# Kernel tuning notes

Measured on AMD Instinct MI355X. Metric: run time of the kernel, lower is better.

Reference implementation:

```python
import jax, jax.numpy as jnp
import numpy as np

FSIZE = 5
PAD = FSIZE // 2


def _conv(mosaick, filts):
    # mosaick [B,1,H,W], filts [f,f,K] -> responses [B,K,H,W].
    # Cross-correlation with edge-clamped boundary (Halide clamp semantics).
    x = jnp.pad(mosaick, ((0, 0), (0, 0), (PAD, PAD), (PAD, PAD)), mode='edge')
    k = jnp.transpose(filts, (2, 0, 1))[:, None, :, :]  # [K,1,f,f] OIHW
    return jax.lax.conv_general_dilated(
        x, k, window_strides=(1, 1), padding='VALID',
        dimension_numbers=('NCHW', 'OIHW', 'NCHW'))


def setup_inputs() -> dict:
    key = jax.random.key(0)
    k1, k2, k3 = jax.random.split(key, 3)
    B, H, W, K, f = 16, 512, 512, 8, FSIZE
    std = 1.0 / (f * f)  # matches normal_(0, 1/(fsize*fsize))
    return {
        'mosaick': jax.random.normal(k1, (B, 1, H, W), dtype=jnp.float32),
        'sel_filts': jax.random.normal(k2, (f, f, K), dtype=jnp.float32) * std,
        'green_filts': jax.random.normal(k3, (f, f, K), dtype=jnp.float32) * std,
    }


def reference(mosaick, sel_filts, green_filts):
    # Per-pixel soft filter selection over K candidate green-interpolation filters.
    sel = _conv(mosaick, sel_filts)      # [B,K,H,W] selection scores
    grn = _conv(mosaick, green_filts)    # [B,K,H,W] candidate green estimates
    w = jax.nn.softmax(sel, axis=1)      # softmax over filter bank
    interp = jnp.sum(w * grn, axis=1, keepdims=True)  # [B,1,H,W]
    # GRBG Bayer: green where row parity == col parity; copy known greens.
    H, W = mosaick.shape[-2], mosaick.shape[-1]
    yy = jnp.arange(H)[:, None]
    xx = jnp.arange(W)[None, :]
    is_green = (yy % 2) == (xx % 2)      # [H,W] bool
    # Output green channel only (module returns output[:, 1:2, ...]).
    return jnp.where(is_green, mosaick, interp)
```

## Files before the change

kernel.cpp:

```cpp
#include <hip/hip_runtime.h>


typedef float f32x4 __attribute__((ext_vector_type(4)));
typedef short s16x8 __attribute__((ext_vector_type(8)));

#define HH 512
#define WW 512
#define TW 64
#define TH 16
#define RS 80
#define NROW 20
#define NEL 72

__device__ __forceinline__ unsigned short bf16rne(float x) {
    unsigned u = __float_as_uint(x);
    u += 0x7fffu + ((u >> 16) & 1u);
    return (unsigned short)(u >> 16);
}
__device__ __forceinline__ int pk2(float hi, float lo) {
    return (int)((((unsigned)bf16rne(hi)) << 16) | (unsigned)bf16rne(lo));
}
__device__ __forceinline__ float hi16(int v) { return __uint_as_float(((unsigned)v) & 0xffff0000u); }
__device__ __forceinline__ float lo16(int v) { return __uint_as_float(((unsigned)v) << 16); }

__global__ __launch_bounds__(256) void demosaick_kernel(
    const float* __restrict__ mos,
    const float* __restrict__ sf,
    const float* __restrict__ gf,
    float* __restrict__ out)
{
    __shared__ alignas(16) unsigned short tileS[NROW * RS];

    const int tid   = threadIdx.x;
    const int bx    = blockIdx.x;
    const int by    = blockIdx.y;
    const int bimg  = blockIdx.z;
    const int tileX = bx * TW;
    const int tileY = by * TH;
    const float* img = mos + (size_t)bimg * HH * WW;

    const bool interior = (bx >= 1) && (bx <= 6) && (by >= 1) && (by <= 30);
    if (interior) {
        if (tid < 180) {
            int r = tid / 9, s = tid - 9 * r;
            const float2* src = (const float2*)(img + (size_t)(tileY - 2 + r) * WW
                                                + (tileX - 2 + 8 * s));
            float2 v0 = src[0], v1 = src[1], v2 = src[2], v3 = src[3];
            int4 d;
            d.x = pk2(v0.y, v0.x);
            d.y = pk2(v1.y, v1.x);
            d.z = pk2(v2.y, v2.x);
            d.w = pk2(v3.y, v3.x);
            *(int4*)&tileS[r * RS + 8 * s] = d;
        }
    } else {
        for (int i = tid; i < NROW * NEL; i += 256) {
            int r = i / NEL, e = i - NEL * r;
            int gy = min(max(tileY - 2 + r, 0), HH - 1);
            int gx = min(max(tileX - 2 + e, 0), WW - 1);
            tileS[r * RS + e] = bf16rne(img[(size_t)gy * WW + gx]);
        }
    }

    const int lane = tid & 63;
    const int w    = tid >> 6;
    const int ch   = lane & 15;
    const int q    = lane >> 4;

    float fv1[5], fv2[5];
#pragma unroll
    for (int dx = 0; dx < 5; ++dx) {
        int t1 = (q * 5 + dx) * 8;
        fv1[dx] = (ch < 8) ? sf[t1 + ch] : gf[t1 + ch - 8];
        int t2 = (20 + dx) * 8;
        fv2[dx] = (q == 0) ? ((ch < 8) ? sf[t2 + ch] : gf[t2 + ch - 8]) : 0.f;
    }
    s16x8 A1[2], A2[2];
#pragma unroll
    for (int p = 0; p < 2; ++p) {
#pragma unroll
        for (int j = 0; j < 8; ++j) {
            int dx = j - p;
            bool ok = (dx >= 0) && (dx <= 4);
            A1[p][j] = ok ? (short)bf16rne(fv1[ok ? dx : 0]) : (short)0;
            A2[p][j] = ok ? (short)bf16rne(fv2[ok ? dx : 0]) : (short)0;
        }
    }

    __syncthreads();

    const int* tb = (const int*)tileS;
    float* outp = out + (size_t)bimg * HH * WW;

#pragma unroll
    for (int i = 0; i < 4; ++i) {
        const int rloc = 4 * w + i;
        const int p    = 1 - (i & 1);
        const int y    = tileY + rloc;
#pragma unroll
        for (int G = 0; G < 2; ++G) {
            int bi1 = (rloc + q) * (RS / 2) + (lane & 15) + 16 * G;
            union { int4 i; s16x8 s; } b1, b2;
            b1.i.x = tb[bi1];     b1.i.y = tb[bi1 + 1];
            b1.i.z = tb[bi1 + 2]; b1.i.w = tb[bi1 + 3];
            int bi2 = (rloc + 4) * (RS / 2) + (lane & 15) + 16 * G;
            b2.i.x = tb[bi2];     b2.i.y = tb[bi2 + 1];
            b2.i.z = tb[bi2 + 2]; b2.i.w = tb[bi2 + 3];

            f32x4 acc = __builtin_amdgcn_mfma_f32_16x16x32_bf16(
                            A1[p], b1.s, (f32x4)(0.f), 0, 0, 0);
            acc = __builtin_amdgcn_mfma_f32_16x16x32_bf16(
                            A2[p], b2.s, acc, 0, 0, 0);

            int d0 = pk2(acc[0], acc[1]);
            int d1 = pk2(acc[2], acc[3]);
            int e0 = __shfl_xor(d0, 32);
            int e1 = __shfl_xor(d1, 32);
            float g0 = hi16(e0), g1 = lo16(e0), g2 = hi16(e1), g3 = lo16(e1);

            float x0 = __expf(acc[0]);
            float x1 = __expf(acc[1]);
            float x2 = __expf(acc[2]);
            float x3 = __expf(acc[3]);
            float den4 = (x0 + x1) + (x2 + x3);
            float num4 = fmaf(x0, g0, fmaf(x1, g1, fmaf(x2, g2, x3 * g3)));

            int nd  = pk2(num4, den4);
            int nd2 = __shfl_xor(nd, 16);
            float num = num4 + hi16(nd2);
            float den = den4 + lo16(nd2);
            float interp = num / den;

            if (lane < 16) {
                int xbase = tileX + 32 * G + 2 * lane;
                int xg    = xbase + (1 - p);
                float green = img[(size_t)y * WW + xg];
                float2 st;
                st.x = p ? green : interp;
                st.y = p ? interp : green;
                *(float2*)(outp + (size_t)y * WW + xbase) = st;
            }
        }
    }
}

extern "C" void kernel_launch(void* const* d_in, const int* in_sizes, int n_in,
                              void* d_out, int out_size, void* d_ws, size_t ws_size,
                              hipStream_t stream) {
    const float* mos = (const float*)d_in[0];
    const float* sf  = (const float*)d_in[1];
    const float* gf  = (const float*)d_in[2];
    float* out = (float*)d_out;

    const int B = in_sizes[0] / (HH * WW);

    dim3 grid(WW / TW, HH / TH, B);
    dim3 block(256);
    demosaick_kernel<<<grid, block, 0, stream>>>(mos, sf, gf, out);
}
```

Before: 90.06 us.

## Switch to 32x32x16 MFMA with interleaved sel/green channels and row-pair B reuse

Replaces the 16x16x32 MFMA formulation with 32x32x16 bf16 MFMAs. The A matrix rows interleave selection and green filter channels, so a lane's accumulator holds adjacent sel/green pairs and the cross-lane shuffle of green values goes away. Each row pair now shares one set of B fragments loaded from LDS for both parity rows. This cuts LDS reads and shuffles per output, at the cost of more MFMA issues, since each 32x32 product is half-empty and needs three instructions per row.

```diff
diff --git a/kernel.cpp b/kernel.cpp
--- a/kernel.cpp
+++ b/kernel.cpp
@@ -1,8 +1,8 @@
 #include <hip/hip_runtime.h>
 
 
-typedef float f32x4 __attribute__((ext_vector_type(4)));
-typedef short s16x8 __attribute__((ext_vector_type(8)));
+typedef float f32x16 __attribute__((ext_vector_type(16)));
+typedef short s16x8  __attribute__((ext_vector_type(8)));
 
 #define HH 512
 #define WW 512
@@ -64,26 +64,31 @@
 
     const int lane = tid & 63;
     const int w    = tid >> 6;
-    const int ch   = lane & 15;
-    const int q    = lane >> 4;
+    const int n    = lane & 31;
+    const int h    = lane >> 5;
+    const int mm   = n;
+    const int c    = mm >> 1;
+    const bool tg  = mm & 1;
+    const bool chok = mm < 16;
+    const float* fb = tg ? gf : sf;
 
-    float fv1[5], fv2[5];
+    s16x8 Aa0 = {0,0,0,0,0,0,0,0}, Ab0 = Aa0, Ac0 = Aa0;
+    s16x8 Aa1 = Aa0, Ab1 = Aa0, Ac1 = Aa0;
 #pragma unroll
-    for (int dx = 0; dx < 5; ++dx) {
-        int t1 = (q * 5 + dx) * 8;
-        fv1[dx] = (ch < 8) ? sf[t1 + ch] : gf[t1 + ch - 8];
-        int t2 = (20 + dx) * 8;
-        fv2[dx] = (q == 0) ? ((ch < 8) ? sf[t2 + ch] : gf[t2 + ch - 8]) : 0.f;
-    }
-    s16x8 A1[2], A2[2];
-#pragma unroll
-    for (int p = 0; p < 2; ++p) {
-#pragma unroll
-        for (int j = 0; j < 8; ++j) {
-            int dx = j - p;
-            bool ok = (dx >= 0) && (dx <= 4);
-            A1[p][j] = ok ? (short)bf16rne(fv1[ok ? dx : 0]) : (short)0;
-            A2[p][j] = ok ? (short)bf16rne(fv2[ok ? dx : 0]) : (short)0;
+    for (int j = 0; j < 8; ++j) {
+        const int dx0 = j - 1;
+        if (dx0 >= 0 && dx0 < 5 && chok) {
+            Aa0[j] = (short)bf16rne(fb[((h)     * 5 + dx0) * 8 + c]);
+            Ab0[j] = (short)bf16rne(fb[((2 + h) * 5 + dx0) * 8 + c]);
+            if (h == 0)
+                Ac0[j] = (short)bf16rne(fb[(4 * 5 + dx0) * 8 + c]);
+        }
+        const int dx1 = j;
+        if (dx1 < 5 && chok) {
+            if (h == 1)
+                Aa1[j] = (short)bf16rne(fb[(0 * 5 + dx1) * 8 + c]);
+            Ab1[j] = (short)bf16rne(fb[((1 + h) * 5 + dx1) * 8 + c]);
+            Ac1[j] = (short)bf16rne(fb[((3 + h) * 5 + dx1) * 8 + c]);
         }
     }
 
@@ -93,52 +98,66 @@
     float* outp = out + (size_t)bimg * HH * WW;
 
 #pragma unroll
-    for (int i = 0; i < 4; ++i) {
-        const int rloc = 4 * w + i;
-        const int p    = 1 - (i & 1);
-        const int y    = tileY + rloc;
+    for (int pp = 0; pp < 2; ++pp) {
+        const int Rl = 4 * w + 2 * pp;
+        const int y  = tileY + Rl;
+        const int ia = (Rl + h) * 40 + n;
+
+        union { int4 v; s16x8 s; } Ba, Bb, Bc;
+        Ba.v.x = tb[ia];       Ba.v.y = tb[ia + 1];
+        Ba.v.z = tb[ia + 2];   Ba.v.w = tb[ia + 3];
+        Bb.v.x = tb[ia + 80];  Bb.v.y = tb[ia + 81];
+        Bb.v.z = tb[ia + 82];  Bb.v.w = tb[ia + 83];
+        Bc.v.x = tb[ia + 160]; Bc.v.y = tb[ia + 161];
+        Bc.v.z = tb[ia + 162]; Bc.v.w = tb[ia + 163];
+
+        f32x16 acc = (f32x16)(0.f);
+        acc = __builtin_amdgcn_mfma_f32_32x32x16_bf16(Aa0, Ba.s, acc, 0, 0, 0);
+        acc = __builtin_amdgcn_mfma_f32_32x32x16_bf16(Ab0, Bb.s, acc, 0, 0, 0);
+        acc = __builtin_amdgcn_mfma_f32_32x32x16_bf16(Ac0, Bc.s, acc, 0, 0, 0);
+        {
+            float den = 0.f, num = 0.f;
 #pragma unroll
-        for (int G = 0; G < 2; ++G) {
-            int bi1 = (rloc + q) * (RS / 2) + (lane & 15) + 16 * G;
-            union { int4 i; s16x8 s; } b1, b2;
-            b1.i.x = tb[bi1];     b1.i.y = tb[bi1 + 1];
-            b1.i.z = tb[bi1 + 2]; b1.i.w = tb[bi1 + 3];
-            int bi2 = (rloc + 4) * (RS / 2) + (lane & 15) + 16 * G;
-            b2.i.x = tb[bi2];     b2.i.y = tb[bi2 + 1];
-            b2.i.z = tb[bi2 + 2]; b2.i.w = tb[bi2 + 3];
+            for (int j = 0; j < 4; ++j) {
+                float e = __expf(acc[2 * j]);
+                den += e;
+                num = fmaf(e, acc[2 * j + 1], num);
+            }
+            int nd  = pk2(num, den);
+            int nd2 = __shfl_xor(nd, 32);
+            num += hi16(nd2);
+            den += lo16(nd2);
+            const float interp = num / den;
+            if (h == 0) {
+                const int x0 = tileX + 2 * n;
+                const float green = img[(size_t)y * WW + x0];
+                float2 st; st.x = green; st.y = interp;
+                *(float2*)(outp + (size_t)y * WW + x0) = st;
+            }
+        }
 
-            f32x4 acc = __builtin_amdgcn_mfma_f32_16x16x32_bf16(
-                            A1[p], b1.s, (f32x4)(0.f), 0, 0, 0);
-            acc = __builtin_amdgcn_mfma_f32_16x16x32_bf16(
-                            A2[p], b2.s, acc, 0, 0, 0);
-
-            int d0 = pk2(acc[0], acc[1]);
-            int d1 = pk2(acc[2], acc[3]);
-            int e0 = __shfl_xor(d0, 32);
-            int e1 = __shfl_xor(d1, 32);
-            float g0 = hi16(e0), g1 = lo16(e0), g2 = hi16(e1), g3 = lo16(e1);
-
-            float x0 = __expf(acc[0]);
-            float x1 = __expf(acc[1]);
-            float x2 = __expf(acc[2]);
-            float x3 = __expf(acc[3]);
-            float den4 = (x0 + x1) + (x2 + x3);
-            float num4 = fmaf(x0, g0, fmaf(x1, g1, fmaf(x2, g2, x3 * g3)));
-
-            int nd  = pk2(num4, den4);
-            int nd2 = __shfl_xor(nd, 16);
-            float num = num4 + hi16(nd2);
-            float den = den4 + lo16(nd2);
-            float interp = num / den;
-
-            if (lane < 16) {
-                int xbase = tileX + 32 * G + 2 * lane;
-                int xg    = xbase + (1 - p);
-                float green = img[(size_t)y * WW + xg];
-                float2 st;
-                st.x = p ? green : interp;
-                st.y = p ? interp : green;
-                *(float2*)(outp + (size_t)y * WW + xbase) = st;
+        f32x16 acc2 = (f32x16)(0.f);
+        acc2 = __builtin_amdgcn_mfma_f32_32x32x16_bf16(Aa1, Ba.s, acc2, 0, 0, 0);
+        acc2 = __builtin_amdgcn_mfma_f32_32x32x16_bf16(Ab1, Bb.s, acc2, 0, 0, 0);
+        acc2 = __builtin_amdgcn_mfma_f32_32x32x16_bf16(Ac1, Bc.s, acc2, 0, 0, 0);
+        {
+            float den = 0.f, num = 0.f;
+#pragma unroll
+            for (int j = 0; j < 4; ++j) {
+                float e = __expf(acc2[2 * j]);
+                den += e;
+                num = fmaf(e, acc2[2 * j + 1], num);
+            }
+            int nd  = pk2(num, den);
+            int nd2 = __shfl_xor(nd, 32);
+            num += hi16(nd2);
+            den += lo16(nd2);
+            const float interp = num / den;
+            if (h == 0) {
+                const int x0 = tileX + 2 * n;
+                const float green = img[(size_t)(y + 1) * WW + x0 + 1];
+                float2 st; st.x = interp; st.y = green;
+                *(float2*)(outp + (size_t)(y + 1) * WW + x0) = st;
             }
         }
     }
```

After: 89.97 us. About the same (-0.1%).
